# Performance work log

Hardware: AMD Instinct MI355X
Metric: run time of the kernel (lower is better)

## Reference

```python
import jax, jax.numpy as jnp
import numpy as np

FEATURE_MAPS = [38, 19, 10, 5, 3, 1]
NUM_ANCHORS = [4, 6, 6, 6, 4, 4]
SCALES = (0.2, 0.9)
RATIOS = np.array([1.0, 1.0, 2.0, 3.0, 0.5, 1.0 / 3.0])
BACKGROUND_ID = 0
EPS = 1e-6


def _generate_anchors():
    """Replicates AnchorManager._generate_anchors: order is (i, j, k)."""
    all_anchors = []
    for size, n in zip(FEATURE_MAPS, NUM_ANCHORS):
        scales = np.linspace(SCALES[0], SCALES[1], n)
        ratios = RATIOS[:n]
        rs = np.sqrt(ratios)
        w = scales * rs          # [n]
        h = scales / rs          # [n]
        cy = (np.arange(size) + 0.5) / size  # i -> rows (varies slowest)
        cx = (np.arange(size) + 0.5) / size  # j -> cols
        grid = np.zeros((size, size, n, 4), dtype=np.float64)
        grid[..., 0] = cx[None, :, None]
        grid[..., 1] = cy[:, None, None]
        grid[..., 2] = w[None, None, :]
        grid[..., 3] = h[None, None, :]
        all_anchors.append(grid.reshape(-1, 4))
    return np.concatenate(all_anchors).astype(np.float32)  # [A, 4] cxcywh


def _cxcywh_to_xyxy(b):
    cxy, wh = b[..., :2], b[..., 2:]
    return jnp.concatenate([cxy - wh / 2, cxy + wh / 2], axis=-1)


def _xyxy_to_cxcywh(b):
    xy1, xy2 = b[..., :2], b[..., 2:]
    return jnp.concatenate([(xy1 + xy2) / 2, xy2 - xy1], axis=-1)


def setup_inputs() -> dict:
    key = jax.random.key(0)
    k1, k2, k3 = jax.random.split(key, 3)
    B, N = 64, 100
    # valid normalized xyxy gt boxes
    xy = jax.random.uniform(k1, (B, N, 2), dtype=jnp.float32) * 0.8
    wh = jax.random.uniform(k2, (B, N, 2), dtype=jnp.float32) * 0.19 + 0.01
    gt_boxes = jnp.concatenate([xy, xy + wh], axis=-1)
    gt_labels = jax.random.randint(k3, (B, N), 1, 81, dtype=jnp.int64 if jax.config.jax_enable_x64 else jnp.int32).astype(jnp.int32)
    anchors_cxcywh = jnp.asarray(_generate_anchors())          # [A, 4]
    anchors_xyxy = _cxcywh_to_xyxy(anchors_cxcywh)             # [A, 4]
    return {
        "gt_labels": gt_labels,
        "gt_boxes": gt_boxes,
        "anchors_cxcywh": anchors_cxcywh,
        "anchors_xyxy": anchors_xyxy,
    }


def _iou(anchors_xyxy, gt_boxes):
    # anchors_xyxy: [A,4], gt_boxes: [B,N,4] -> iou [B,A,N]
    a = anchors_xyxy[None, :, None, :]   # [1,A,1,4]
    g = gt_boxes[:, None, :, :]          # [B,1,N,4]
    lt = jnp.maximum(a[..., :2], g[..., :2])
    rb = jnp.minimum(a[..., 2:], g[..., 2:])
    wh = jnp.clip(rb - lt, 0.0)
    inter = wh[..., 0] * wh[..., 1]
    area_a = (a[..., 2] - a[..., 0]) * (a[..., 3] - a[..., 1])
    area_g = (g[..., 2] - g[..., 0]) * (g[..., 3] - g[..., 1])
    return (inter / (area_a + area_g - inter)).astype(jnp.float32)


def reference(gt_labels, gt_boxes, anchors_cxcywh, anchors_xyxy):
    B, N = gt_boxes.shape[0], gt_boxes.shape[1]
    A = anchors_cxcywh.shape[0]

    gt_boxes_coco = _xyxy_to_cxcywh(gt_boxes)                  # [B,N,4]
    ious = _iou(anchors_xyxy, gt_boxes)                        # [B,A,N]

    anchors_gt = jnp.max(ious, axis=-1)                        # [B,A]
    anchors_gt_idx = jnp.argmax(ious, axis=-1)                 # [B,A]
    gt_anchors_idx = jnp.argmax(ious, axis=-2)                 # [B,N] best anchor per gt

    # force-match: each gt claims its best anchor
    b_idx = jnp.arange(B)[:, None]
    range_n = jnp.broadcast_to(jnp.arange(N), (B, N))
    anchors_gt_idx = anchors_gt_idx.at[b_idx, gt_anchors_idx].set(range_n)
    anchors_gt = anchors_gt.at[b_idx, gt_anchors_idx].set(2.0)

    pos_mask = anchors_gt > 0.5                                # [B,A]

    matched_gtb = jnp.take_along_axis(gt_boxes_coco, anchors_gt_idx[..., None], axis=1)  # [B,A,4]
    matched_labels = jnp.take_along_axis(gt_labels, anchors_gt_idx, axis=1)              # [B,A]
    encoded_labels = jnp.where(pos_mask, matched_labels, BACKGROUND_ID)

    anc = anchors_cxcywh[None]                                 # [1,A,4]
    enc_cxy = (matched_gtb[..., :2] - anc[..., :2]) / anc[..., 2:]
    enc_wh = jnp.log((matched_gtb[..., 2:] + EPS) / (anc[..., 2:] + EPS))
    encoded = jnp.concatenate([enc_cxy, enc_wh], axis=-1)      # [B,A,4]

    return encoded_labels, encoded, pos_mask
```

## Files before the change

### kernel.cpp

```cpp
#include <hip/hip_runtime.h>
#include <math.h>

#pragma clang fp contract(off)


#define AA 8732
#define NN 100
#define BB 64
#define EPS_F 1e-6f
#define OVR_FLAG 0x10000

__constant__ int FM_SIZE[6] = {38, 19, 10, 5, 3, 1};
__constant__ int FM_NF[6]   = {4, 6, 6, 6, 4, 4};
__constant__ int FM_OFF[6]  = {0, 5776, 7942, 8542, 8692, 8728};

__device__ __forceinline__ float iou_exact(float4 an, float4 g,
                                           float area_a, float area_g) {
    float ltx = fmaxf(an.x, g.x);
    float lty = fmaxf(an.y, g.y);
    float rbx = fminf(an.z, g.z);
    float rby = fminf(an.w, g.w);
    float w = fmaxf(rbx - ltx, 0.0f);
    float h = fmaxf(rby - lty, 0.0f);
    float inter = w * h;
    return inter / (area_a + area_g - inter);
}

__global__ void prior_kernel(const float4* __restrict__ gt_boxes,
                             const float4* __restrict__ anchors_xyxy,
                             unsigned* __restrict__ prior) {
    const int b = blockIdx.x;
    const int n = threadIdx.x;
    if (n >= NN) return;
    float4 g = gt_boxes[b * NN + n];
    float area_g = (g.z - g.x) * (g.w - g.y);
    float cx = (g.x + g.z) * 0.5f;
    float cy = (g.y + g.w) * 0.5f;
    float best = 0.0f;
    for (int f = 0; f < 6; f++) {
        int s = FM_SIZE[f];
        int j = (int)(cx * (float)s); j = j < s - 1 ? j : s - 1;
        int i = (int)(cy * (float)s); i = i < s - 1 ? i : s - 1;
        int base = FM_OFF[f] + (i * s + j) * FM_NF[f];
        for (int k = 0; k < FM_NF[f]; k++) {
            float4 an = anchors_xyxy[base + k];
            float area_a = (an.z - an.x) * (an.w - an.y);
            best = fmaxf(best, iou_exact(an, g, area_a, area_g));
        }
    }
    prior[b * NN + n] = __float_as_uint(best);
}

__global__ __launch_bounds__(256) void iou_pass_kernel(
        const float4* __restrict__ gt_boxes,
        const float4* __restrict__ anchors_xyxy,
        const unsigned* __restrict__ prior,
        unsigned long long* __restrict__ colmax,
        float* __restrict__ out_val,
        int* __restrict__ out_slot)
{
    const int b = blockIdx.y;
    const int tid = threadIdx.x;
    const int a = blockIdx.x * 256 + tid;
    const bool valid = (a < AA);
    const int ac = valid ? a : (AA - 1);

    __shared__ float4   sg[NN];
    __shared__ float    sarea[NN];
    __shared__ unsigned scurhi[NN];

    if (tid < NN) {
        float4 g = gt_boxes[b * NN + tid];
        sg[tid] = g;
        sarea[tid] = (g.z - g.x) * (g.w - g.y);
        unsigned p = prior[b * NN + tid];
        scurhi[tid] = p > 1u ? p : 1u;
    }
    __syncthreads();

    const float4 axy = anchors_xyxy[ac];
    const float area_a = (axy.z - axy.x) * (axy.w - axy.y);

    float bv = -1.0f;
    int bi = 0;

    #pragma unroll 4
    for (int n = 0; n < NN; n++) {
        float iou = iou_exact(axy, sg[n], area_a, sarea[n]);

        if (iou > bv) { bv = iou; bi = n; }

        unsigned qb = valid ? __float_as_uint(iou) : 0u;
        if (__any((int)(qb >= scurhi[n]))) {
            unsigned m = qb;
            #pragma unroll
            for (int off = 32; off > 0; off >>= 1) {
                unsigned o = __shfl_xor(m, off);
                m = o > m ? o : m;
            }
            unsigned long long ball = __ballot((int)(qb == m));
            int leader = __ffsll((long long)ball) - 1;
            if ((tid & 63) == leader) {
                unsigned long long v =
                    (((unsigned long long)m) << 32) | (unsigned)(AA - a);
                atomicMax(colmax + b * NN + n, v);
                atomicMax(&scurhi[n], m);
            }
        }
    }

    if (valid) {
        const size_t base = (size_t)b * AA + a;
        out_val[base] = bv;
        out_slot[base] = bi;
    }
}

__global__ void scatter_kernel(const unsigned long long* __restrict__ colmax,
                               int* __restrict__ out_slot) {
    const int b = blockIdx.x;
    const int n = threadIdx.x;
    if (n < NN) {
        unsigned long long v = colmax[b * NN + n];
        unsigned low = (unsigned)(v & 0xFFFFFFFFull);
        if (low >= 1u && low <= (unsigned)AA) {
            int idx = AA - (int)low;
            atomicMax(&out_slot[(size_t)b * AA + idx], OVR_FLAG + n);
        }
    }
}

__global__ __launch_bounds__(256) void encode_kernel(
        const int* __restrict__ gt_labels,
        const float4* __restrict__ gt_boxes,
        const float4* __restrict__ anchors_cxcywh,
        float* __restrict__ out)
{
    const int b = blockIdx.y;
    const int tid = threadIdx.x;
    const int a = blockIdx.x * 256 + tid;

    __shared__ float4 sg[NN];
    __shared__ int    slab[NN];
    if (tid < NN) {
        sg[tid]   = gt_boxes[b * NN + tid];
        slab[tid] = gt_labels[b * NN + tid];
    }
    __syncthreads();
    if (a >= AA) return;

    const size_t BA = (size_t)BB * AA;
    const size_t base = (size_t)b * AA + a;

    float bv = out[base];
    int s = ((const int*)(out + 5 * BA))[base];

    int idx; float val;
    if (s >= OVR_FLAG) { idx = s - OVR_FLAG; val = 2.0f; }
    else               { idx = s;            val = bv;   }
    const bool pos = val > 0.5f;

    const float4 g = sg[idx];
    const float gcx = (g.x + g.z) * 0.5f;
    const float gcy = (g.y + g.w) * 0.5f;
    const float gw  = g.z - g.x;
    const float gh  = g.w - g.y;

    const float4 anc = anchors_cxcywh[a];
    const float ecx = (gcx - anc.x) / anc.z;
    const float ecy = (gcy - anc.y) / anc.w;
    const float ew  = logf((gw + EPS_F) / (anc.z + EPS_F));
    const float eh  = logf((gh + EPS_F) / (anc.w + EPS_F));

    out[base] = pos ? (float)slab[idx] : 0.0f;
    ((float4*)(out + BA))[base] = make_float4(ecx, ecy, ew, eh);
    out[5 * BA + base] = pos ? 1.0f : 0.0f;
}

extern "C" void kernel_launch(void* const* d_in, const int* in_sizes, int n_in,
                              void* d_out, int out_size, void* d_ws, size_t ws_size,
                              hipStream_t stream) {
    const int*    gt_labels    = (const int*)d_in[0];
    const float4* gt_boxes     = (const float4*)d_in[1];
    const float4* anchors_cxcy = (const float4*)d_in[2];
    const float4* anchors_xyxy = (const float4*)d_in[3];
    float* out = (float*)d_out;

    const size_t BA = (size_t)BB * AA;
    unsigned long long* colmax = (unsigned long long*)(out + BA);
    int* slot = (int*)(out + 5 * BA);
    unsigned* prior = (unsigned*)d_ws;

    hipMemsetAsync(colmax, 0, (size_t)BB * NN * sizeof(unsigned long long), stream);

    prior_kernel<<<BB, 128, 0, stream>>>(gt_boxes, anchors_xyxy, prior);

    dim3 grid((AA + 255) / 256, BB);
    iou_pass_kernel<<<grid, 256, 0, stream>>>(gt_boxes, anchors_xyxy, prior,
                                              colmax, out, slot);
    scatter_kernel<<<BB, 128, 0, stream>>>(colmax, slot);
    encode_kernel<<<grid, 256, 0, stream>>>(gt_labels, gt_boxes, anchors_cxcy, out);
}
```

Measured before the change: 133.4 us.

## Two-pass IoU with approximate reciprocal screening and exact recompute on candidates

The IoU pass first screens all gt boxes using a fast approximate reciprocal and records a per-wave bitmask of candidates that could be the row max or could beat the column threshold. A second pass recomputes the exact IoU division only for those candidates and does the wave reduction and atomics only there. It also drops the memset by having the prior kernel seed colmax with the prior value. This trades a second loop and slack thresholds for fewer exact divides and less divergent shuffle work, and its correctness depends on the deflation margin covering the reciprocal error.

```diff
diff --git a/kernel.cpp b/kernel.cpp
--- a/kernel.cpp
+++ b/kernel.cpp
@@ -9,6 +9,7 @@
 #define BB 64
 #define EPS_F 1e-6f
 #define OVR_FLAG 0x10000
+#define DEFL 0.9999995f
 
 __constant__ int FM_SIZE[6] = {38, 19, 10, 5, 3, 1};
 __constant__ int FM_NF[6]   = {4, 6, 6, 6, 4, 4};
@@ -28,7 +29,8 @@
 
 __global__ void prior_kernel(const float4* __restrict__ gt_boxes,
                              const float4* __restrict__ anchors_xyxy,
-                             unsigned* __restrict__ prior) {
+                             float* __restrict__ prior,
+                             unsigned long long* __restrict__ colmax) {
     const int b = blockIdx.x;
     const int n = threadIdx.x;
     if (n >= NN) return;
@@ -48,13 +50,14 @@
             best = fmaxf(best, iou_exact(an, g, area_a, area_g));
         }
     }
-    prior[b * NN + n] = __float_as_uint(best);
+    prior[b * NN + n] = best;
+    colmax[b * NN + n] = ((unsigned long long)__float_as_uint(best)) << 32;
 }
 
 __global__ __launch_bounds__(256) void iou_pass_kernel(
         const float4* __restrict__ gt_boxes,
         const float4* __restrict__ anchors_xyxy,
-        const unsigned* __restrict__ prior,
+        const float* __restrict__ prior,
         unsigned long long* __restrict__ colmax,
         float* __restrict__ out_val,
         int* __restrict__ out_slot)
@@ -65,46 +68,111 @@
     const bool valid = (a < AA);
     const int ac = valid ? a : (AA - 1);
 
-    __shared__ float4   sg[NN];
-    __shared__ float    sarea[NN];
-    __shared__ unsigned scurhi[NN];
+    __shared__ float4 sg[NN];
+    __shared__ float  sarea[NN];
+    __shared__ float  scurf[NN];
 
     if (tid < NN) {
         float4 g = gt_boxes[b * NN + tid];
         sg[tid] = g;
         sarea[tid] = (g.z - g.x) * (g.w - g.y);
-        unsigned p = prior[b * NN + tid];
-        scurhi[tid] = p > 1u ? p : 1u;
+        scurf[tid] = prior[b * NN + tid] * DEFL;
     }
     __syncthreads();
 
     const float4 axy = anchors_xyxy[ac];
     const float area_a = (axy.z - axy.x) * (axy.w - axy.y);
 
-    float bv = -1.0f;
+    float am = 0.0f;
+    unsigned long long wmLo = 0ull, wmHi = 0ull;
+
+    #pragma unroll 4
+    for (int n = 0; n < 64; n++) {
+        float4 g = sg[n];
+        float ag = sarea[n];
+        float ltx = fmaxf(axy.x, g.x);
+        float lty = fmaxf(axy.y, g.y);
+        float rbx = fminf(axy.z, g.z);
+        float rby = fminf(axy.w, g.w);
+        float w = fmaxf(rbx - ltx, 0.0f);
+        float h = fmaxf(rby - lty, 0.0f);
+        float inter = w * h;
+        float uni = area_a + ag - inter;
+        float qa = inter * __builtin_amdgcn_rcpf(uni);
+        bool r = (qa > 0.0f) && (qa >= am * DEFL);
+        bool c = valid && (qa >= scurf[n]);
+        am = fmaxf(am, qa);
+        unsigned long long wf = (unsigned long long)__any((int)(r | c));
+        wmLo |= wf << n;
+    }
+    #pragma unroll 4
+    for (int n = 64; n < NN; n++) {
+        float4 g = sg[n];
+        float ag = sarea[n];
+        float ltx = fmaxf(axy.x, g.x);
+        float lty = fmaxf(axy.y, g.y);
+        float rbx = fminf(axy.z, g.z);
+        float rby = fminf(axy.w, g.w);
+        float w = fmaxf(rbx - ltx, 0.0f);
+        float h = fmaxf(rby - lty, 0.0f);
+        float inter = w * h;
+        float uni = area_a + ag - inter;
+        float qa = inter * __builtin_amdgcn_rcpf(uni);
+        bool r = (qa > 0.0f) && (qa >= am * DEFL);
+        bool c = valid && (qa >= scurf[n]);
+        am = fmaxf(am, qa);
+        unsigned long long wf = (unsigned long long)__any((int)(r | c));
+        wmHi |= wf << (n - 64);
+    }
+
+    const float amthr = am * DEFL;
+    float bv = 0.0f;
     int bi = 0;
 
-    #pragma unroll 4
-    for (int n = 0; n < NN; n++) {
-        float iou = iou_exact(axy, sg[n], area_a, sarea[n]);
-
-        if (iou > bv) { bv = iou; bi = n; }
-
-        unsigned qb = valid ? __float_as_uint(iou) : 0u;
-        if (__any((int)(qb >= scurhi[n]))) {
-            unsigned m = qb;
-            #pragma unroll
-            for (int off = 32; off > 0; off >>= 1) {
-                unsigned o = __shfl_xor(m, off);
-                m = o > m ? o : m;
-            }
-            unsigned long long ball = __ballot((int)(qb == m));
-            int leader = __ffsll((long long)ball) - 1;
-            if ((tid & 63) == leader) {
-                unsigned long long v =
-                    (((unsigned long long)m) << 32) | (unsigned)(AA - a);
-                atomicMax(colmax + b * NN + n, v);
-                atomicMax(&scurhi[n], m);
+    #pragma unroll 1
+    for (int half = 0; half < 2; half++) {
+        unsigned long long wm = half ? wmHi : wmLo;
+        const int nbase = half ? 64 : 0;
+        while (wm) {
+            int n = __builtin_ctzll(wm) + nbase;
+            wm &= wm - 1;
+            float4 g = sg[n];
+            float ag = sarea[n];
+            float ltx = fmaxf(axy.x, g.x);
+            float lty = fmaxf(axy.y, g.y);
+            float rbx = fminf(axy.z, g.z);
+            float rby = fminf(axy.w, g.w);
+            float w = fmaxf(rbx - ltx, 0.0f);
+            float h = fmaxf(rby - lty, 0.0f);
+            float inter = w * h;
+            float uni = area_a + ag - inter;
+            float qa = inter * __builtin_amdgcn_rcpf(uni);
+            bool rc = (qa > 0.0f) && (qa >= amthr);
+            bool cc = valid && (qa >= scurf[n]);
+            if (__any((int)(rc | cc))) {
+                float iou = inter / uni;
+                if (iou > bv) { bv = iou; bi = n; }
+                if (__any((int)cc)) {
+                    unsigned qb = valid ? __float_as_uint(iou) : 0u;
+                    unsigned m = qb;
+                    #pragma unroll
+                    for (int off = 32; off > 0; off >>= 1) {
+                        unsigned o = __shfl_xor(m, off);
+                        m = o > m ? o : m;
+                    }
+                    unsigned long long ball = __ballot((int)(qb == m && m > 0u));
+                    if (ball) {
+                        int leader = __ffsll((long long)ball) - 1;
+                        if ((tid & 63) == leader) {
+                            unsigned long long v =
+                                (((unsigned long long)m) << 32) |
+                                (unsigned long long)(unsigned)(AA - a);
+                            atomicMax(colmax + b * NN + n, v);
+                            atomicMax((unsigned*)&scurf[n],
+                                      __float_as_uint(__uint_as_float(m) * DEFL));
+                        }
+                    }
+                }
             }
         }
     }
@@ -189,11 +257,9 @@
     const size_t BA = (size_t)BB * AA;
     unsigned long long* colmax = (unsigned long long*)(out + BA);
     int* slot = (int*)(out + 5 * BA);
-    unsigned* prior = (unsigned*)d_ws;
-
-    hipMemsetAsync(colmax, 0, (size_t)BB * NN * sizeof(unsigned long long), stream);
-
-    prior_kernel<<<BB, 128, 0, stream>>>(gt_boxes, anchors_xyxy, prior);
+    float* prior = (float*)d_ws;
+
+    prior_kernel<<<BB, 128, 0, stream>>>(gt_boxes, anchors_xyxy, prior, colmax);
 
     dim3 grid((AA + 255) / 256, BB);
     iou_pass_kernel<<<grid, 256, 0, stream>>>(gt_boxes, anchors_xyxy, prior,
```

Result: slower. 152.5 us (+14.3%).

## Fuse prior computation into IoU pass and filter candidates via approximate reciprocal

Applied to the files above, without the earlier changes.

The prior-bound kernel is removed and its work is folded into each IoU block's shared-memory setup. The main loop now computes IoU with the fast hardware reciprocal and records candidate bitmasks for the row max and for column updates. Exact division and the wave-level column reduction with atomics run only on flagged candidates, with a slightly relaxed threshold so the result stays exact. This cuts per-element divisions and per-iteration wave votes, but every block now repeats the prior work and divergent candidate loops are added.

```diff
diff --git a/kernel.cpp b/kernel.cpp
--- a/kernel.cpp
+++ b/kernel.cpp
@@ -9,52 +9,47 @@
 #define BB 64
 #define EPS_F 1e-6f
 #define OVR_FLAG 0x10000
+#define DEFL 0.9999995f
 
 __constant__ int FM_SIZE[6] = {38, 19, 10, 5, 3, 1};
 __constant__ int FM_NF[6]   = {4, 6, 6, 6, 4, 4};
 __constant__ int FM_OFF[6]  = {0, 5776, 7942, 8542, 8692, 8728};
 
-__device__ __forceinline__ float iou_exact(float4 an, float4 g,
-                                           float area_a, float area_g) {
-    float ltx = fmaxf(an.x, g.x);
-    float lty = fmaxf(an.y, g.y);
-    float rbx = fminf(an.z, g.z);
-    float rby = fminf(an.w, g.w);
+__device__ __forceinline__ void geom(const float4 axy, const float4 g,
+                                     float area_a, float ag,
+                                     float& inter, float& uni) {
+    float ltx = fmaxf(axy.x, g.x);
+    float lty = fmaxf(axy.y, g.y);
+    float rbx = fminf(axy.z, g.z);
+    float rby = fminf(axy.w, g.w);
     float w = fmaxf(rbx - ltx, 0.0f);
     float h = fmaxf(rby - lty, 0.0f);
-    float inter = w * h;
-    return inter / (area_a + area_g - inter);
-}
-
-__global__ void prior_kernel(const float4* __restrict__ gt_boxes,
-                             const float4* __restrict__ anchors_xyxy,
-                             unsigned* __restrict__ prior) {
-    const int b = blockIdx.x;
-    const int n = threadIdx.x;
-    if (n >= NN) return;
-    float4 g = gt_boxes[b * NN + n];
-    float area_g = (g.z - g.x) * (g.w - g.y);
-    float cx = (g.x + g.z) * 0.5f;
-    float cy = (g.y + g.w) * 0.5f;
-    float best = 0.0f;
-    for (int f = 0; f < 6; f++) {
-        int s = FM_SIZE[f];
-        int j = (int)(cx * (float)s); j = j < s - 1 ? j : s - 1;
-        int i = (int)(cy * (float)s); i = i < s - 1 ? i : s - 1;
-        int base = FM_OFF[f] + (i * s + j) * FM_NF[f];
-        for (int k = 0; k < FM_NF[f]; k++) {
-            float4 an = anchors_xyxy[base + k];
-            float area_a = (an.z - an.x) * (an.w - an.y);
-            best = fmaxf(best, iou_exact(an, g, area_a, area_g));
-        }
-    }
-    prior[b * NN + n] = __float_as_uint(best);
+    inter = w * h;
+    uni = area_a + ag - inter;
+}
+
+template <int N0, int N1>
+__device__ __forceinline__ void phaseA(const float4 axy, float area_a,
+                                       bool valid,
+                                       const float4* sg, const float* sarea,
+                                       const float* scurf,
+                                       float& am, unsigned& rm, unsigned& cm) {
+    #pragma unroll 4
+    for (int n = N0; n < N1; n++) {
+        float inter, uni;
+        geom(axy, sg[n], area_a, sarea[n], inter, uni);
+        float qa = inter * __builtin_amdgcn_rcpf(uni);
+        bool r = (qa > 0.0f) && (qa >= am * DEFL);
+        bool c = valid && (qa >= scurf[n]);
+        am = fmaxf(am, qa);
+        rm |= (r ? 1u : 0u) << (n - N0);
+        cm |= (c ? 1u : 0u) << (n - N0);
+    }
 }
 
 __global__ __launch_bounds__(256) void iou_pass_kernel(
         const float4* __restrict__ gt_boxes,
         const float4* __restrict__ anchors_xyxy,
-        const unsigned* __restrict__ prior,
         unsigned long long* __restrict__ colmax,
         float* __restrict__ out_val,
         int* __restrict__ out_slot)
@@ -65,46 +60,108 @@
     const bool valid = (a < AA);
     const int ac = valid ? a : (AA - 1);
 
-    __shared__ float4   sg[NN];
-    __shared__ float    sarea[NN];
-    __shared__ unsigned scurhi[NN];
+    __shared__ float4 sg[NN];
+    __shared__ float  sarea[NN];
+    __shared__ float  scurf[NN];
 
     if (tid < NN) {
         float4 g = gt_boxes[b * NN + tid];
         sg[tid] = g;
-        sarea[tid] = (g.z - g.x) * (g.w - g.y);
-        unsigned p = prior[b * NN + tid];
-        scurhi[tid] = p > 1u ? p : 1u;
+        float ag = (g.z - g.x) * (g.w - g.y);
+        sarea[tid] = ag;
+        float cx = (g.x + g.z) * 0.5f;
+        float cy = (g.y + g.w) * 0.5f;
+        float best = 0.0f;
+        for (int f = 0; f < 6; f++) {
+            int s = FM_SIZE[f];
+            int j = (int)(cx * (float)s); j = j < s - 1 ? j : s - 1;
+            int i = (int)(cy * (float)s); i = i < s - 1 ? i : s - 1;
+            int base = FM_OFF[f] + (i * s + j) * FM_NF[f];
+            for (int k = 0; k < FM_NF[f]; k++) {
+                float4 an = anchors_xyxy[base + k];
+                float area_a = (an.z - an.x) * (an.w - an.y);
+                float inter, uni;
+                geom(an, g, area_a, ag, inter, uni);
+                best = fmaxf(best, inter * __builtin_amdgcn_rcpf(uni));
+            }
+        }
+        scurf[tid] = best * DEFL;
     }
     __syncthreads();
 
     const float4 axy = anchors_xyxy[ac];
     const float area_a = (axy.z - axy.x) * (axy.w - axy.y);
 
-    float bv = -1.0f;
+    float am = 0.0f;
+    unsigned rm0 = 0, rm1 = 0, rm2 = 0, rm3 = 0;
+    unsigned cm0 = 0, cm1 = 0, cm2 = 0, cm3 = 0;
+    phaseA<0, 32>(axy, area_a, valid, sg, sarea, scurf, am, rm0, cm0);
+    phaseA<32, 64>(axy, area_a, valid, sg, sarea, scurf, am, rm1, cm1);
+    phaseA<64, 96>(axy, area_a, valid, sg, sarea, scurf, am, rm2, cm2);
+    phaseA<96, NN>(axy, area_a, valid, sg, sarea, scurf, am, rm3, cm3);
+
+    const float amthr = am * DEFL;
+    float bv = 0.0f;
     int bi = 0;
-
-    #pragma unroll 4
-    for (int n = 0; n < NN; n++) {
-        float iou = iou_exact(axy, sg[n], area_a, sarea[n]);
-
-        if (iou > bv) { bv = iou; bi = n; }
-
-        unsigned qb = valid ? __float_as_uint(iou) : 0u;
-        if (__any((int)(qb >= scurhi[n]))) {
-            unsigned m = qb;
+    {
+        unsigned rms[4] = {rm0, rm1, rm2, rm3};
+        #pragma unroll
+        for (int h = 0; h < 4; h++) {
+            unsigned m = rms[h];
+            const int nb = h * 32;
+            while (m) {
+                int n = __builtin_ctz(m) + nb;
+                m &= m - 1;
+                float inter, uni;
+                geom(axy, sg[n], area_a, sarea[n], inter, uni);
+                float qa = inter * __builtin_amdgcn_rcpf(uni);
+                if (qa > 0.0f && qa >= amthr) {
+                    float iou = inter / uni;
+                    if (iou > bv) { bv = iou; bi = n; }
+                }
+            }
+        }
+    }
+
+    {
+        unsigned cms[4] = {cm0, cm1, cm2, cm3};
+        #pragma unroll
+        for (int h = 0; h < 4; h++) {
+            unsigned wc = cms[h];
             #pragma unroll
-            for (int off = 32; off > 0; off >>= 1) {
-                unsigned o = __shfl_xor(m, off);
-                m = o > m ? o : m;
-            }
-            unsigned long long ball = __ballot((int)(qb == m));
-            int leader = __ffsll((long long)ball) - 1;
-            if ((tid & 63) == leader) {
-                unsigned long long v =
-                    (((unsigned long long)m) << 32) | (unsigned)(AA - a);
-                atomicMax(colmax + b * NN + n, v);
-                atomicMax(&scurhi[n], m);
+            for (int off = 32; off > 0; off >>= 1)
+                wc |= __shfl_xor(wc, off);
+            const int nb = h * 32;
+            while (wc) {
+                int n = __builtin_ctz(wc) + nb;
+                wc &= wc - 1;
+                float inter, uni;
+                geom(axy, sg[n], area_a, sarea[n], inter, uni);
+                float qa = inter * __builtin_amdgcn_rcpf(uni);
+                bool cc = valid && (qa >= scurf[n]);
+                if (__any((int)cc)) {
+                    float iou = inter / uni;
+                    unsigned qb = cc ? __float_as_uint(iou) : 0u;
+                    unsigned mm = qb;
+                    #pragma unroll
+                    for (int off = 32; off > 0; off >>= 1) {
+                        unsigned o = __shfl_xor(mm, off);
+                        mm = o > mm ? o : mm;
+                    }
+                    unsigned long long ball =
+                        __ballot((int)(qb == mm && mm > 0u));
+                    if (ball) {
+                        int leader = __ffsll((long long)ball) - 1;
+                        if ((tid & 63) == leader) {
+                            unsigned long long v =
+                                (((unsigned long long)mm) << 32) |
+                                (unsigned long long)(unsigned)(AA - a);
+                            atomicMax(colmax + b * NN + n, v);
+                            atomicMax((unsigned*)&scurf[n],
+                                __float_as_uint(__uint_as_float(mm) * DEFL));
+                        }
+                    }
+                }
             }
         }
     }
@@ -189,15 +246,14 @@
     const size_t BA = (size_t)BB * AA;
     unsigned long long* colmax = (unsigned long long*)(out + BA);
     int* slot = (int*)(out + 5 * BA);
-    unsigned* prior = (unsigned*)d_ws;
-
-    hipMemsetAsync(colmax, 0, (size_t)BB * NN * sizeof(unsigned long long), stream);
-
-    prior_kernel<<<BB, 128, 0, stream>>>(gt_boxes, anchors_xyxy, prior);
+
+    (void)hipMemsetAsync(colmax, 0,
+                         (size_t)BB * NN * sizeof(unsigned long long), stream);
 
     dim3 grid((AA + 255) / 256, BB);
-    iou_pass_kernel<<<grid, 256, 0, stream>>>(gt_boxes, anchors_xyxy, prior,
-                                              colmax, out, slot);
+    iou_pass_kernel<<<grid, 256, 0, stream>>>(gt_boxes, anchors_xyxy, colmax,
+                                              out, slot);
     scatter_kernel<<<BB, 128, 0, stream>>>(colmax, slot);
-    encode_kernel<<<grid, 256, 0, stream>>>(gt_labels, gt_boxes, anchors_cxcy, out);
-}
+    encode_kernel<<<grid, 256, 0, stream>>>(gt_labels, gt_boxes, anchors_cxcy,
+                                            out);
+}
```

Measured after the change: 145.5 us. +9.0%, slower.
